# Performance work log

Hardware: AMD Instinct MI355X
Metric: run time of the kernel (lower is better)

The kernel has to match this reference:

```python
import jax, jax.numpy as jnp
import numpy as np

B, P = 128, 16384
DT = 0.01
L1 = L2 = M1 = M2 = 1.0
SCALE_AUX = 0.1


def setup_inputs() -> dict:
    key = jax.random.key(0)
    prev_latents = jax.random.normal(key, (B, P, 6), dtype=jnp.float32)
    return {"prev_latents": prev_latents, "time": 1}


def reference(prev_latents, time):
    # time != 0 branch of Bootstrap_Proposal.forward.
    # prev_latents: [B, P, 6] = [torque1, torque2, angle1, angle2(elbow), vel1, vel2]
    t2 = prev_latents[..., 3]                  # elbow angle, [B, P]
    c = jnp.cos(t2)
    # 2x2 inertia tensor entries (symmetric)
    d00 = L1 ** 2 * M1 / 3 + M2 * (3 * L1 ** 2 + 3 * L1 * L2 * c + L2 ** 2) / 3
    d01 = L2 * M2 * (3 * L1 * c + 2 * L2) / 6
    d11 = jnp.full_like(t2, L2 ** 2 * M2 / 3)
    # Newton's 2nd law: accel = D^{-1} @ (torque - h - c), with h = c = 0.
    # Analytic 2x2 inverse (same math as torch.inverse on 2x2 blocks).
    det = d00 * d11 - d01 * d01
    tq1 = prev_latents[..., 0]
    tq2 = prev_latents[..., 1]
    a1 = (d11 * tq1 - d01 * tq2) / det
    a2 = (-d01 * tq1 + d00 * tq2) / det
    zeros = jnp.zeros_like(t2)
    # ax = [0, 0, vel1, vel2, accel1, accel2]
    ax = jnp.stack([zeros, zeros, prev_latents[..., 4], prev_latents[..., 5], a1, a2], axis=-1)
    mean = prev_latents + DT * ax              # loc of the MultivariateNormal, [B, P, 6]
    return mean
```

## Files before the change

kernel.cpp:

```cpp
#include <hip/hip_runtime.h>


#define DT 0.01f

__device__ __forceinline__ void particle_step(
    float tq1, float tq2, float th1, float th2, float v1, float v2,
    float& m0, float& m1, float& m2, float& m3, float& m4, float& m5) {
    const float c    = cosf(th2);
    const float rden = 1.0f / (16.0f - 9.0f * c * c);
    const float s    = 6.0f * (3.0f * c + 2.0f);
    const float a1   = (12.0f * tq1 - s * tq2) * rden;
    const float a2   = (12.0f * (5.0f + 3.0f * c) * tq2 - s * tq1) * rden;
    m0 = tq1;
    m1 = tq2;
    m2 = th1 + DT * v1;
    m3 = th2 + DT * v2;
    m4 = v1 + DT * a1;
    m5 = v2 + DT * a2;
}

__global__ void __launch_bounds__(256)
bootstrap_proposal_kernel(const float4* __restrict__ in4,
                          float4* __restrict__ out4,
                          long long nvec) {
    __shared__ float4 lds[768];
    const int t = threadIdx.x;
    const long long base = (long long)blockIdx.x * 768;

#pragma unroll
    for (int k = 0; k < 3; ++k) {
        const long long idx = base + k * 256 + t;
        if (idx < nvec) lds[k * 256 + t] = in4[idx];
    }
    __syncthreads();

    const float4 v0 = lds[3 * t + 0];
    const float4 v1 = lds[3 * t + 1];
    const float4 v2 = lds[3 * t + 2];

    float4 o0, o1, o2;
    particle_step(v0.x, v0.y, v0.z, v0.w, v1.x, v1.y,
                  o0.x, o0.y, o0.z, o0.w, o1.x, o1.y);
    particle_step(v1.z, v1.w, v2.x, v2.y, v2.z, v2.w,
                  o1.z, o1.w, o2.x, o2.y, o2.z, o2.w);

    lds[3 * t + 0] = o0;
    lds[3 * t + 1] = o1;
    lds[3 * t + 2] = o2;
    __syncthreads();

#pragma unroll
    for (int k = 0; k < 3; ++k) {
        const long long idx = base + k * 256 + t;
        if (idx < nvec) out4[idx] = lds[k * 256 + t];
    }
}

extern "C" void kernel_launch(void* const* d_in, const int* in_sizes, int n_in,
                              void* d_out, int out_size, void* d_ws, size_t ws_size,
                              hipStream_t stream) {
    const float* in = (const float*)d_in[0];
    float* out = (float*)d_out;
    const long long nvec = (long long)out_size / 4;
    const int grid = (int)((nvec + 767) / 768);
    bootstrap_proposal_kernel<<<grid, 256, 0, stream>>>(
        (const float4*)in, (float4*)out, nvec);
}
```

Baseline: 20.75 us.

## Use per-wave LDS tiles, nontemporal memory ops, and two tiles per thread

Each wave now stages its own 192-vector tile in LDS, so the block-wide barriers become per-wave lgkmcnt waits. Global loads and stores use nontemporal builtins. Each thread processes two tiles, which doubles the work per block and halves the grid. The custom waitcnt relies on the wave-private LDS regions being written and read only by the same wave, and halving the grid reduces parallelism for this memory-bound streaming kernel.

```diff
diff --git a/kernel.cpp b/kernel.cpp
--- a/kernel.cpp
+++ b/kernel.cpp
@@ -3,56 +3,88 @@
 
 #define DT 0.01f
 
-__device__ __forceinline__ void particle_step(
-    float tq1, float tq2, float th1, float th2, float v1, float v2,
-    float& m0, float& m1, float& m2, float& m3, float& m4, float& m5) {
+typedef float f4 __attribute__((ext_vector_type(4)));
+
+#define LGKM0() asm volatile("s_waitcnt lgkmcnt(0)" ::: "memory")
+
+struct Six { float m0, m1, m2, m3, m4, m5; };
+
+__device__ __forceinline__ Six particle_step(
+    float tq1, float tq2, float th1, float th2, float v1, float v2) {
     const float c    = cosf(th2);
     const float rden = 1.0f / (16.0f - 9.0f * c * c);
     const float s    = 6.0f * (3.0f * c + 2.0f);
     const float a1   = (12.0f * tq1 - s * tq2) * rden;
     const float a2   = (12.0f * (5.0f + 3.0f * c) * tq2 - s * tq1) * rden;
-    m0 = tq1;
-    m1 = tq2;
-    m2 = th1 + DT * v1;
-    m3 = th2 + DT * v2;
-    m4 = v1 + DT * a1;
-    m5 = v2 + DT * a2;
+    Six r;
+    r.m0 = tq1;
+    r.m1 = tq2;
+    r.m2 = th1 + DT * v1;
+    r.m3 = th2 + DT * v2;
+    r.m4 = v1 + DT * a1;
+    r.m5 = v2 + DT * a2;
+    return r;
+}
+
+__device__ __forceinline__ void pair_step(const f4 v0, const f4 v1,
+                                          const f4 v2, f4& o0,
+                                          f4& o1, f4& o2) {
+    const Six p = particle_step(v0.x, v0.y, v0.z, v0.w, v1.x, v1.y);
+    const Six q = particle_step(v1.z, v1.w, v2.x, v2.y, v2.z, v2.w);
+    f4 t0, t1, t2;
+    t0.x = p.m0; t0.y = p.m1; t0.z = p.m2; t0.w = p.m3;
+    t1.x = p.m4; t1.y = p.m5; t1.z = q.m0; t1.w = q.m1;
+    t2.x = q.m2; t2.y = q.m3; t2.z = q.m4; t2.w = q.m5;
+    o0 = t0; o1 = t1; o2 = t2;
 }
 
 __global__ void __launch_bounds__(256)
-bootstrap_proposal_kernel(const float4* __restrict__ in4,
-                          float4* __restrict__ out4,
+bootstrap_proposal_kernel(const f4* __restrict__ in4,
+                          f4* __restrict__ out4,
                           long long nvec) {
-    __shared__ float4 lds[768];
-    const int t = threadIdx.x;
-    const long long base = (long long)blockIdx.x * 768;
+    __shared__ f4 lds[1536];
+    const int t    = threadIdx.x;
+    const int w    = t >> 6;
+    const int lane = t & 63;
+    const long long base = (long long)blockIdx.x * 1536;
+
+    const int tile0 = w * 192;
+    const int tile1 = 768 + w * 192;
 
 #pragma unroll
-    for (int k = 0; k < 3; ++k) {
-        const long long idx = base + k * 256 + t;
-        if (idx < nvec) lds[k * 256 + t] = in4[idx];
+    for (int j = 0; j < 3; ++j) {
+        const long long i0 = base + tile0 + j * 64 + lane;
+        const long long i1 = base + tile1 + j * 64 + lane;
+        if (i0 < nvec) lds[tile0 + j * 64 + lane] = __builtin_nontemporal_load(&in4[i0]);
+        if (i1 < nvec) lds[tile1 + j * 64 + lane] = __builtin_nontemporal_load(&in4[i1]);
     }
-    __syncthreads();
+    LGKM0();
 
-    const float4 v0 = lds[3 * t + 0];
-    const float4 v1 = lds[3 * t + 1];
-    const float4 v2 = lds[3 * t + 2];
+    const f4 a0 = lds[tile0 + 3 * lane + 0];
+    const f4 a1 = lds[tile0 + 3 * lane + 1];
+    const f4 a2 = lds[tile0 + 3 * lane + 2];
+    const f4 b0 = lds[tile1 + 3 * lane + 0];
+    const f4 b1 = lds[tile1 + 3 * lane + 1];
+    const f4 b2 = lds[tile1 + 3 * lane + 2];
 
-    float4 o0, o1, o2;
-    particle_step(v0.x, v0.y, v0.z, v0.w, v1.x, v1.y,
-                  o0.x, o0.y, o0.z, o0.w, o1.x, o1.y);
-    particle_step(v1.z, v1.w, v2.x, v2.y, v2.z, v2.w,
-                  o1.z, o1.w, o2.x, o2.y, o2.z, o2.w);
+    f4 oa0, oa1, oa2, ob0, ob1, ob2;
+    pair_step(a0, a1, a2, oa0, oa1, oa2);
+    pair_step(b0, b1, b2, ob0, ob1, ob2);
 
-    lds[3 * t + 0] = o0;
-    lds[3 * t + 1] = o1;
-    lds[3 * t + 2] = o2;
-    __syncthreads();
+    lds[tile0 + 3 * lane + 0] = oa0;
+    lds[tile0 + 3 * lane + 1] = oa1;
+    lds[tile0 + 3 * lane + 2] = oa2;
+    lds[tile1 + 3 * lane + 0] = ob0;
+    lds[tile1 + 3 * lane + 1] = ob1;
+    lds[tile1 + 3 * lane + 2] = ob2;
+    LGKM0();
 
 #pragma unroll
-    for (int k = 0; k < 3; ++k) {
-        const long long idx = base + k * 256 + t;
-        if (idx < nvec) out4[idx] = lds[k * 256 + t];
+    for (int j = 0; j < 3; ++j) {
+        const long long i0 = base + tile0 + j * 64 + lane;
+        const long long i1 = base + tile1 + j * 64 + lane;
+        if (i0 < nvec) __builtin_nontemporal_store(lds[tile0 + j * 64 + lane], &out4[i0]);
+        if (i1 < nvec) __builtin_nontemporal_store(lds[tile1 + j * 64 + lane], &out4[i1]);
     }
 }
 
@@ -62,7 +94,7 @@
     const float* in = (const float*)d_in[0];
     float* out = (float*)d_out;
     const long long nvec = (long long)out_size / 4;
-    const int grid = (int)((nvec + 767) / 768);
+    const int grid = (int)((nvec + 1535) / 1536);
     bootstrap_proposal_kernel<<<grid, 256, 0, stream>>>(
-        (const float4*)in, (float4*)out, nvec);
+        (const f4*)in, (f4*)out, nvec);
 }
```

New measurement: 21.53 us. +3.7%, slower.

## Replace LDS transpose with per-float4 neighbor loads and nontemporal stores

Applied to the files above, without the earlier changes.

Each thread now handles one float4 of output and loads its own float4 plus one neighboring float4 (chosen by index mod 3) to reconstruct the particle fields it needs. This removes the shared-memory staging, both barriers and 64-bit indexing. Nontemporal stores are used for the output. The cost is one extra global load per thread (mostly cache hits), cosine work computed redundantly per float4, and a mod-3 computation.

```diff
diff --git a/kernel.cpp b/kernel.cpp
--- a/kernel.cpp
+++ b/kernel.cpp
@@ -3,57 +3,39 @@
 
 #define DT 0.01f
 
-__device__ __forceinline__ void particle_step(
-    float tq1, float tq2, float th1, float th2, float v1, float v2,
-    float& m0, float& m1, float& m2, float& m3, float& m4, float& m5) {
+typedef float f4 __attribute__((ext_vector_type(4)));
+
+__global__ void __launch_bounds__(256)
+bootstrap_proposal_kernel(const f4* __restrict__ in4,
+                          f4* __restrict__ out4,
+                          int nvec) {
+    const int idx = blockIdx.x * 256 + threadIdx.x;
+    if (idx >= nvec) return;
+
+    const int phase = idx % 3;
+    const f4 a = in4[idx];
+    const f4 b = in4[idx + ((phase == 0) ? 1 : -1)];
+
+    const float th2  = (phase == 1) ? b.w : a.y;
+    const float tq1  = (phase == 1) ? b.x : b.z;
+    const float tq2  = (phase == 1) ? b.y : b.w;
     const float c    = cosf(th2);
     const float rden = 1.0f / (16.0f - 9.0f * c * c);
     const float s    = 6.0f * (3.0f * c + 2.0f);
-    const float a1   = (12.0f * tq1 - s * tq2) * rden;
-    const float a2   = (12.0f * (5.0f + 3.0f * c) * tq2 - s * tq1) * rden;
-    m0 = tq1;
-    m1 = tq2;
-    m2 = th1 + DT * v1;
-    m3 = th2 + DT * v2;
-    m4 = v1 + DT * a1;
-    m5 = v2 + DT * a2;
-}
+    const float acc1 = (12.0f * tq1 - s * tq2) * rden;
+    const float acc2 = (12.0f * (5.0f + 3.0f * c) * tq2 - s * tq1) * rden;
 
-__global__ void __launch_bounds__(256)
-bootstrap_proposal_kernel(const float4* __restrict__ in4,
-                          float4* __restrict__ out4,
-                          long long nvec) {
-    __shared__ float4 lds[768];
-    const int t = threadIdx.x;
-    const long long base = (long long)blockIdx.x * 768;
+    const float sx = (phase == 0) ? 0.0f : ((phase == 1) ? acc1 : a.z);
+    const float sy = (phase == 0) ? 0.0f : ((phase == 1) ? acc2 : a.w);
+    const float sz = (phase == 0) ? b.x  : ((phase == 1) ? 0.0f : acc1);
+    const float sw = (phase == 0) ? b.y  : ((phase == 1) ? 0.0f : acc2);
 
-#pragma unroll
-    for (int k = 0; k < 3; ++k) {
-        const long long idx = base + k * 256 + t;
-        if (idx < nvec) lds[k * 256 + t] = in4[idx];
-    }
-    __syncthreads();
-
-    const float4 v0 = lds[3 * t + 0];
-    const float4 v1 = lds[3 * t + 1];
-    const float4 v2 = lds[3 * t + 2];
-
-    float4 o0, o1, o2;
-    particle_step(v0.x, v0.y, v0.z, v0.w, v1.x, v1.y,
-                  o0.x, o0.y, o0.z, o0.w, o1.x, o1.y);
-    particle_step(v1.z, v1.w, v2.x, v2.y, v2.z, v2.w,
-                  o1.z, o1.w, o2.x, o2.y, o2.z, o2.w);
-
-    lds[3 * t + 0] = o0;
-    lds[3 * t + 1] = o1;
-    lds[3 * t + 2] = o2;
-    __syncthreads();
-
-#pragma unroll
-    for (int k = 0; k < 3; ++k) {
-        const long long idx = base + k * 256 + t;
-        if (idx < nvec) out4[idx] = lds[k * 256 + t];
-    }
+    f4 o;
+    o.x = a.x + DT * sx;
+    o.y = a.y + DT * sy;
+    o.z = a.z + DT * sz;
+    o.w = a.w + DT * sw;
+    __builtin_nontemporal_store(o, &out4[idx]);
 }
 
 extern "C" void kernel_launch(void* const* d_in, const int* in_sizes, int n_in,
@@ -61,8 +43,8 @@
                               hipStream_t stream) {
     const float* in = (const float*)d_in[0];
     float* out = (float*)d_out;
-    const long long nvec = (long long)out_size / 4;
-    const int grid = (int)((nvec + 767) / 768);
+    const int nvec = out_size / 4;
+    const int grid = (nvec + 255) / 256;
     bootstrap_proposal_kernel<<<grid, 256, 0, stream>>>(
-        (const float4*)in, (float4*)out, nvec);
+        (const f4*)in, (f4*)out, nvec);
 }
```

New measurement: 20.70 us. About the same (-0.2%).
